# Performance work log

Hardware: AMD Instinct MI355X
Metric: run time of the kernel (lower is better)

The kernel has to match this reference:

```python
import jax, jax.numpy as jnp
import numpy as np

N, E, D, R, G, C = 100000, 600000, 128, 4, 256, 16
EPS = 1e-5

def _rgcn(x, src, dst, edge_type, w_rel, w_root, b):
    # out_i = x_i @ W_root + b + sum_r mean_{j in N_r(i)} x_j @ W_r  (PyG RGCNConv, aggr='mean')
    x_src = x[src]                                   # [E, D] gather
    out = x @ w_root + b                             # [N, D]
    for r in range(R):
        m = (edge_type == r).astype(x.dtype)         # [E]
        msg = (x_src @ w_rel[r]) * m[:, None]        # [E, D]
        agg = jax.ops.segment_sum(msg, dst, num_segments=N)
        cnt = jax.ops.segment_sum(m, dst, num_segments=N)
        out = out + agg / jnp.maximum(cnt, 1.0)[:, None]
    return out

def _bn_eval(x, gamma, beta, mean, var):
    return (x - mean) * jax.lax.rsqrt(var + EPS) * gamma + beta

def setup_inputs() -> dict:
    key = jax.random.key(0)
    ks = jax.random.split(key, 12)
    x = jax.random.normal(ks[0], (N, D), dtype=jnp.float32)
    edge_index = jax.random.randint(ks[1], (2, E), 0, N)
    edge_type = jax.random.randint(ks[2], (E,), 0, R)
    batch = jnp.sort(jax.random.randint(ks[3], (N,), 0, G))
    s = 1.0 / np.sqrt(D)
    conv_rel_w = jax.random.normal(ks[4], (3, R, D, D), dtype=jnp.float32) * s
    conv_root_w = jax.random.normal(ks[5], (3, D, D), dtype=jnp.float32) * s
    conv_bias = jnp.zeros((3, D), dtype=jnp.float32)
    bn_gamma = jnp.ones((2, D), dtype=jnp.float32)
    bn_beta = jnp.zeros((2, D), dtype=jnp.float32)
    bn_mean = jax.random.normal(ks[6], (2, D), dtype=jnp.float32) * 0.1
    bn_var = jax.random.uniform(ks[7], (2, D), minval=0.5, maxval=1.5, dtype=jnp.float32)
    cls_w1 = jax.random.normal(ks[8], (D, D // 2), dtype=jnp.float32) * s
    cls_b1 = jnp.zeros((D // 2,), dtype=jnp.float32)
    cls_w2 = jax.random.normal(ks[9], (D // 2, C), dtype=jnp.float32) / np.sqrt(D // 2)
    cls_b2 = jnp.zeros((C,), dtype=jnp.float32)
    return {"x": x, "edge_index": edge_index, "edge_type": edge_type, "batch": batch,
            "conv_rel_w": conv_rel_w, "conv_root_w": conv_root_w, "conv_bias": conv_bias,
            "bn_gamma": bn_gamma, "bn_beta": bn_beta, "bn_mean": bn_mean, "bn_var": bn_var,
            "cls_w1": cls_w1, "cls_b1": cls_b1, "cls_w2": cls_w2, "cls_b2": cls_b2}

def reference(x, edge_index, edge_type, batch, conv_rel_w, conv_root_w, conv_bias,
              bn_gamma, bn_beta, bn_mean, bn_var, cls_w1, cls_b1, cls_w2, cls_b2):
    src, dst = edge_index[0], edge_index[1]
    prev = None
    h = x
    for i in range(3):
        h_new = _rgcn(h, src, dst, edge_type, conv_rel_w[i], conv_root_w[i], conv_bias[i])
        if prev is not None:
            h_new = h_new + prev  # residual (shapes always match: D==D)
        if i != 2:
            h_new = _bn_eval(h_new, bn_gamma[i], bn_beta[i], bn_mean[i], bn_var[i])
            h_new = jax.nn.elu(h_new)  # alpha=1; dropout inactive in eval
        prev = h_new
        h = h_new
    # global mean pool over graphs
    sums = jax.ops.segment_sum(h, batch, num_segments=G)          # [G, D]
    cnts = jax.ops.segment_sum(jnp.ones((N,), h.dtype), batch, num_segments=G)
    pooled = sums / jnp.maximum(cnts, 1.0)[:, None]
    z = jax.nn.elu(pooled @ cls_w1 + cls_b1)
    logits = z @ cls_w2 + cls_b2
    return jax.nn.log_softmax(logits, axis=-1)
```

## Files before the change

### kernel.cpp

```cpp
#include <hip/hip_runtime.h>
#include <hip/hip_bf16.h>

#define NN 100000
#define EE 600000
#define DD 128
#define GG 256
#define CCL 16

typedef __attribute__((ext_vector_type(8))) short short8;
typedef __attribute__((ext_vector_type(4))) float f32x4;

__global__ __launch_bounds__(256) void sniff_kernel(const void* __restrict__ xraw, int* __restrict__ flag) {
    int t = threadIdx.x;
    const unsigned short* u = (const unsigned short*)xraw;
    int good = 0;
    #pragma unroll
    for (int i = 0; i < 4; i++) {
        unsigned short b = u[t * 4 + i];
        int e = (b >> 7) & 0xFF;
        if (e >= 107 && e <= 130) good++;
    }
    __shared__ int sg[256];
    sg[t] = good;
    __syncthreads();
    for (int s = 128; s > 0; s >>= 1) { if (t < s) sg[t] += sg[t + s]; __syncthreads(); }
    if (t == 0) flag[0] = (sg[0] >= 900) ? 1 : 0;
}

__device__ __forceinline__ float loadf(const void* p, size_t i, int isbf) {
    if (isbf) {
        unsigned short b = ((const unsigned short*)p)[i];
        return __uint_as_float(((unsigned)b) << 16);
    }
    return ((const float*)p)[i];
}

__global__ __launch_bounds__(256) void convx_kernel(const void* __restrict__ xraw, const int* __restrict__ flag,
                                                    __hip_bfloat16* __restrict__ xc) {
    int isbf = flag[0];
    size_t i0 = ((size_t)blockIdx.x * 256 + threadIdx.x) * 8;
    if (i0 >= (size_t)NN * DD) return;
    if (isbf) {
        *(uint4*)(xc + i0) = *(const uint4*)((const __hip_bfloat16*)xraw + i0);
    } else {
        const float* xf = (const float*)xraw;
        #pragma unroll
        for (int j = 0; j < 8; j++) xc[i0 + j] = __float2bfloat16(xf[i0 + j]);
    }
}

__global__ __launch_bounds__(256) void convw_kernel(const void* __restrict__ rel_raw, const void* __restrict__ root_raw,
                                                    const int* __restrict__ flag, __hip_bfloat16* __restrict__ wt) {
    int isbf = flag[0];
    int mat = blockIdx.x;
    int layer = mat / 5, g = mat % 5;
    size_t srcoff = (g == 0) ? (size_t)layer * 16384 : (size_t)(layer * 4 + (g - 1)) * 16384;
    const void* sraw = (g == 0) ? root_raw : rel_raw;
    __hip_bfloat16* dstp = wt + (size_t)mat * 16384;
    for (int idx = threadIdx.x; idx < 16384; idx += 256) {
        int k = idx >> 7, n = idx & 127;
        float v = loadf(sraw, srcoff + (size_t)k * 128 + n, isbf);
        dstp[n * 128 + k] = __float2bfloat16(v);
    }
}

__global__ __launch_bounds__(256) void convp_kernel(const void* bias, const void* bng, const void* bnb,
                                                    const void* bnm, const void* bnv, const void* w1,
                                                    const void* b1, const void* w2, const void* b2,
                                                    const int* __restrict__ flag, float* __restrict__ pf) {
    int isbf = flag[0];
    const void* srcs[9] = {bias, bng, bnb, bnm, bnv, w1, b1, w2, b2};
    const int cnts[9] = {384, 256, 256, 256, 256, 8192, 64, 1024, 16};
    const int offs[9] = {0, 384, 640, 896, 1152, 1408, 9600, 9664, 10688};
    int b = blockIdx.x;
    const void* s = srcs[b];
    int c = cnts[b], o = offs[b];
    for (int i = threadIdx.x; i < c; i += 256) pf[o + i] = loadf(s, i, isbf);
}

__global__ __launch_bounds__(256) void count_kernel(const int* __restrict__ dst, int* __restrict__ cnt) {
    int e = blockIdx.x * 256 + threadIdx.x;
    if (e < EE) atomicAdd(&cnt[dst[e]], 1);
}

__global__ __launch_bounds__(256) void alloc_kernel(const int* __restrict__ cnt, int* __restrict__ counter,
                                                    int* __restrict__ startp, int* __restrict__ wptr) {
    int n = blockIdx.x * 256 + threadIdx.x;
    int lane = threadIdx.x & 63;
    int c = (n < NN) ? cnt[n] : 0;
    int v = c;
    #pragma unroll
    for (int d = 1; d < 64; d <<= 1) {
        int o = __shfl_up(v, d);
        if (lane >= d) v += o;
    }
    int base = 0;
    if (lane == 63) base = atomicAdd(counter, v);
    base = __shfl(base, 63);
    if (n < NN) {
        int s = base + v - c;
        startp[n] = s;
        wptr[n]  = s;
    }
}

__global__ __launch_bounds__(256) void fill_kernel(const int* __restrict__ src, const int* __restrict__ dst,
                                                   const int* __restrict__ et, int* __restrict__ wptr,
                                                   int* __restrict__ elist) {
    int e = blockIdx.x * 256 + threadIdx.x;
    if (e < EE) {
        int d = dst[e];
        int pos = atomicAdd(&wptr[d], 1);
        elist[pos] = src[e] | (et[e] << 17);
    }
}

__global__ __launch_bounds__(256) void agg_kernel(const __hip_bfloat16* __restrict__ h,
                                                  const int* __restrict__ elist,
                                                  const int* __restrict__ startp,
                                                  const int* __restrict__ cnt,
                                                  __hip_bfloat16* __restrict__ xagg) {
    int wid = (blockIdx.x * 256 + threadIdx.x) >> 6;
    int lane = threadIdx.x & 63;
    if (wid >= NN) return;
    int s = startp[wid], c = cnt[wid];
    float a0x=0,a0y=0,a1x=0,a1y=0,a2x=0,a2y=0,a3x=0,a3y=0;
    int c0=0,c1=0,c2=0,c3=0;
    int my = (lane < c) ? elist[s + lane] : 0;
    for (int e = 0; e < c; e++) {
        int packed = (e < 64) ? __shfl(my, e) : elist[s + e];
        int srcn = packed & 0x1FFFF;
        int r = (packed >> 17) & 3;
        __hip_bfloat162 v = ((const __hip_bfloat162*)(h + (size_t)srcn * DD))[lane];
        float vx = __bfloat162float(v.x), vy = __bfloat162float(v.y);
        if (r == 0)      { a0x += vx; a0y += vy; c0++; }
        else if (r == 1) { a1x += vx; a1y += vy; c1++; }
        else if (r == 2) { a2x += vx; a2y += vy; c2++; }
        else             { a3x += vx; a3y += vy; c3++; }
    }
    __hip_bfloat162* out = (__hip_bfloat162*)(xagg + (size_t)wid * 512);
    float i0 = 1.0f / (float)(c0 ? c0 : 1), i1 = 1.0f / (float)(c1 ? c1 : 1);
    float i2 = 1.0f / (float)(c2 ? c2 : 1), i3 = 1.0f / (float)(c3 ? c3 : 1);
    __hip_bfloat162 o;
    o.x = __float2bfloat16(a0x * i0); o.y = __float2bfloat16(a0y * i0); out[lane]       = o;
    o.x = __float2bfloat16(a1x * i1); o.y = __float2bfloat16(a1y * i1); out[64 + lane]  = o;
    o.x = __float2bfloat16(a2x * i2); o.y = __float2bfloat16(a2y * i2); out[128 + lane] = o;
    o.x = __float2bfloat16(a3x * i3); o.y = __float2bfloat16(a3y * i3); out[192 + lane] = o;
}

__global__ __launch_bounds__(256) void gemm_kernel(const __hip_bfloat16* __restrict__ h_in,
                                                   const __hip_bfloat16* __restrict__ xagg,
                                                   const __hip_bfloat16* __restrict__ wt,
                                                   const float* __restrict__ bias,
                                                   const float* __restrict__ bng,
                                                   const float* __restrict__ bnb,
                                                   const float* __restrict__ bnm,
                                                   const float* __restrict__ bnv,
                                                   const __hip_bfloat16* __restrict__ hres,
                                                   __hip_bfloat16* __restrict__ hout,
                                                   int do_bn) {
    __shared__ __align__(16) __hip_bfloat16 Alds[128][136];
    __shared__ __align__(16) __hip_bfloat16 Blds[128][136];
    int t = threadIdx.x;
    int wave = t >> 6, lane = t & 63;
    int quad = lane >> 4, r16 = lane & 15;
    int m0 = blockIdx.x * 128;
    f32x4 acc[2][8];
    #pragma unroll
    for (int i = 0; i < 2; i++)
        #pragma unroll
        for (int j = 0; j < 8; j++) acc[i][j] = (f32x4){0.f, 0.f, 0.f, 0.f};

    for (int g = 0; g < 5; g++) {
        #pragma unroll
        for (int it = 0; it < 8; it++) {
            int sgi = t + it * 256;
            int row = sgi >> 4, seg = sgi & 15;
            int node = m0 + row; if (node >= NN) node = NN - 1;
            const uint4* sp = (g == 0)
                ? (const uint4*)(h_in + (size_t)node * 128)
                : (const uint4*)(xagg + (size_t)node * 512 + (size_t)(g - 1) * 128);
            uint4 val = sp[seg];
            *(uint4*)&Alds[row][seg * 8] = val;
        }
        const uint4* wp = (const uint4*)(wt + (size_t)g * 16384);
        #pragma unroll
        for (int it = 0; it < 8; it++) {
            int sgi = t + it * 256;
            int n = sgi >> 4, seg = sgi & 15;
            uint4 val = wp[n * 16 + seg];
            *(uint4*)&Blds[n][seg * 8] = val;
        }
        __syncthreads();
        #pragma unroll
        for (int kc = 0; kc < 4; kc++) {
            short8 a0 = *(const short8*)&Alds[wave * 32 + r16][kc * 32 + quad * 8];
            short8 a1 = *(const short8*)&Alds[wave * 32 + 16 + r16][kc * 32 + quad * 8];
            #pragma unroll
            for (int nt = 0; nt < 8; nt++) {
                short8 b = *(const short8*)&Blds[nt * 16 + r16][kc * 32 + quad * 8];
                acc[0][nt] = __builtin_amdgcn_mfma_f32_16x16x32_bf16(a0, b, acc[0][nt], 0, 0, 0);
                acc[1][nt] = __builtin_amdgcn_mfma_f32_16x16x32_bf16(a1, b, acc[1][nt], 0, 0, 0);
            }
        }
        __syncthreads();
    }
    #pragma unroll
    for (int nt = 0; nt < 8; nt++) {
        int col = nt * 16 + r16;
        float bv = bias[col];
        float gmul = 0.f, gadd = 0.f;
        if (do_bn) {
            float iva = rsqrtf(bnv[col] + 1e-5f);
            gmul = bng[col] * iva;
            gadd = bnb[col] - bnm[col] * gmul;
        }
        #pragma unroll
        for (int mt = 0; mt < 2; mt++) {
            #pragma unroll
            for (int reg = 0; reg < 4; reg++) {
                int node = m0 + wave * 32 + mt * 16 + quad * 4 + reg;
                if (node >= NN) continue;
                float v = acc[mt][nt][reg] + bv;
                if (hres) v += __bfloat162float(hres[(size_t)node * 128 + col]);
                if (do_bn) {
                    v = v * gmul + gadd;
                    v = v > 0.f ? v : expm1f(v);
                }
                hout[(size_t)node * 128 + col] = __float2bfloat16(v);
            }
        }
    }
}

__global__ __launch_bounds__(256) void pool_kernel(const __hip_bfloat16* __restrict__ h3,
                                                   const int* __restrict__ batch,
                                                   float* __restrict__ pooled) {
    int g = blockIdx.x, t = threadIdx.x;
    int d = t & 127, half = t >> 7;
    int lo = 0, hi = NN;
    while (lo < hi) { int mid = (lo + hi) >> 1; if (batch[mid] < g) lo = mid + 1; else hi = mid; }
    int s0 = lo;
    hi = NN;
    while (lo < hi) { int mid = (lo + hi) >> 1; if (batch[mid] < g + 1) lo = mid + 1; else hi = mid; }
    int s1 = lo;
    float acc = 0.f;
    for (int n = s0 + half; n < s1; n += 2) acc += __bfloat162float(h3[(size_t)n * 128 + d]);
    __shared__ float sd[256];
    sd[t] = acc;
    __syncthreads();
    if (t < 128) {
        int c = s1 - s0;
        pooled[g * 128 + t] = (sd[t] + sd[t + 128]) / (float)(c > 0 ? c : 1);
    }
}

__global__ __launch_bounds__(64) void cls_kernel(const float* __restrict__ pooled,
                                                 const float* __restrict__ pf,
                                                 const int* __restrict__ flag,
                                                 void* __restrict__ out) {
    int g = blockIdx.x, j = threadIdx.x;
    const float* w1 = pf + 1408;
    const float* b1 = pf + 9600;
    const float* w2 = pf + 9664;
    const float* b2 = pf + 10688;
    __shared__ float z[64];
    __shared__ float lg[16];
    const float* p = pooled + g * 128;
    float acc = b1[j];
    for (int d = 0; d < 128; d++) acc += p[d] * w1[d * 64 + j];
    acc = acc > 0.f ? acc : expm1f(acc);
    z[j] = acc;
    __syncthreads();
    if (j < CCL) {
        float l = b2[j];
        for (int k = 0; k < 64; k++) l += z[k] * w2[k * 16 + j];
        lg[j] = l;
    }
    __syncthreads();
    if (j < CCL) {
        float m = lg[0];
        for (int k = 1; k < CCL; k++) m = fmaxf(m, lg[k]);
        float s = 0.f;
        for (int k = 0; k < CCL; k++) s += expf(lg[k] - m);
        float val = lg[j] - m - logf(s);
        if (flag[0]) ((__hip_bfloat16*)out)[g * CCL + j] = __float2bfloat16(val);
        else         ((float*)out)[g * CCL + j] = val;
    }
}

extern "C" void kernel_launch(void* const* d_in, const int* in_sizes, int n_in,
                              void* d_out, int out_size, void* d_ws, size_t ws_size,
                              hipStream_t stream) {
    const void* x_raw    = d_in[0];
    const int* ei        = (const int*)d_in[1];
    const int* et        = (const int*)d_in[2];
    const int* batch     = (const int*)d_in[3];
    const void* rel_raw  = d_in[4];
    const void* root_raw = d_in[5];
    const void* bias_r   = d_in[6];
    const void* bng_r    = d_in[7];
    const void* bnb_r    = d_in[8];
    const void* bnm_r    = d_in[9];
    const void* bnv_r    = d_in[10];
    const void* w1_r     = d_in[11];
    const void* b1_r     = d_in[12];
    const void* w2_r     = d_in[13];
    const void* b2_r     = d_in[14];
    const int* srcp = ei;
    const int* dstp = ei + EE;

    char* ws = (char*)d_ws;
    size_t off = 0;
    auto take = [&](size_t bytes) { size_t r = off; off += (bytes + 1023) & ~(size_t)1023; return r; };
    __hip_bfloat16* xagg = (__hip_bfloat16*)(ws + take((size_t)NN * 512 * 2));
    __hip_bfloat16* xc   = (__hip_bfloat16*)(ws + take((size_t)NN * 128 * 2));
    __hip_bfloat16* hA   = (__hip_bfloat16*)(ws + take((size_t)NN * 128 * 2));
    __hip_bfloat16* hB   = (__hip_bfloat16*)(ws + take((size_t)NN * 128 * 2));
    __hip_bfloat16* hC   = (__hip_bfloat16*)(ws + take((size_t)NN * 128 * 2));
    __hip_bfloat16* wt   = (__hip_bfloat16*)(ws + take((size_t)15 * 16384 * 2));
    float* pf            = (float*)(ws + take((size_t)10704 * 4));
    float* pooled        = (float*)(ws + take((size_t)GG * 128 * 4));
    int* cnt             = (int*)(ws + take((size_t)NN * 4 + 8));
    int* counter         = cnt + NN;
    int* flag            = cnt + NN + 1;
    int* startp          = (int*)(ws + take((size_t)NN * 4));
    int* wptr            = (int*)(ws + take((size_t)NN * 4));
    int* elist           = (int*)(ws + take((size_t)EE * 4));

    hipMemsetAsync(cnt, 0, (size_t)NN * 4 + 4, stream);
    sniff_kernel<<<1, 256, 0, stream>>>(x_raw, flag);
    convx_kernel<<<(NN * DD / 8 + 255) / 256, 256, 0, stream>>>(x_raw, flag, xc);
    convw_kernel<<<15, 256, 0, stream>>>(rel_raw, root_raw, flag, wt);
    convp_kernel<<<9, 256, 0, stream>>>(bias_r, bng_r, bnb_r, bnm_r, bnv_r,
                                        w1_r, b1_r, w2_r, b2_r, flag, pf);
    count_kernel<<<(EE + 255) / 256, 256, 0, stream>>>(dstp, cnt);
    alloc_kernel<<<(NN + 255) / 256, 256, 0, stream>>>(cnt, counter, startp, wptr);
    fill_kernel<<<(EE + 255) / 256, 256, 0, stream>>>(srcp, dstp, et, wptr, elist);

    const __hip_bfloat16* hin = xc;
    __hip_bfloat16* houts[3] = {hA, hB, hC};
    for (int l = 0; l < 3; l++) {
        agg_kernel<<<(NN * 64 + 255) / 256, 256, 0, stream>>>(hin, elist, startp, cnt, xagg);
        int bl = l < 2 ? l : 1;
        gemm_kernel<<<(NN + 127) / 128, 256, 0, stream>>>(
            hin, xagg, wt + (size_t)l * 5 * 16384, pf + l * 128,
            pf + 384 + bl * 128, pf + 640 + bl * 128, pf + 896 + bl * 128, pf + 1152 + bl * 128,
            (l > 0) ? hin : (const __hip_bfloat16*)nullptr, houts[l], (l < 2) ? 1 : 0);
        hin = houts[l];
    }
    pool_kernel<<<GG, 256, 0, stream>>>(houts[2], batch, pooled);
    cls_kernel<<<GG, 64, 0, stream>>>(pooled, pf, flag, (void*)d_out);
}
```

Before: 706.1 us.

## Vectorize aggregation, async-LDS swizzled GEMM with staged epilogue, vectorized pooling

The aggregation kernel now gives each 16-lane group one neighbor edge and reads 16-byte rows, handling two edges per group per iteration. Per-relation sums and counts are combined with cross-lane shuffles instead of one 4-byte load per lane per edge. The GEMM loads its tiles with global_load_lds into a smaller XOR-swizzled LDS buffer over ten K=64 chunks, and precomputes the BN scale and shift in shared memory. Its epilogue is staged through LDS so residual reads and output writes are 16-byte vectors. Pooling and the fp32-to-bf16 conversion are also vectorized. This adds more synchronization points per K chunk and more complex indexing.

```diff
diff --git a/kernel.cpp b/kernel.cpp
--- a/kernel.cpp
+++ b/kernel.cpp
@@ -9,6 +9,26 @@
 
 typedef __attribute__((ext_vector_type(8))) short short8;
 typedef __attribute__((ext_vector_type(4))) float f32x4;
+typedef const __attribute__((address_space(1))) void* gas_t;
+typedef __attribute__((address_space(3))) void* las_t;
+
+__device__ __forceinline__ void async_ld16(const void* g, void* l) {
+    __builtin_amdgcn_global_load_lds((gas_t)g, (las_t)l, 16, 0, 0);
+}
+__device__ __forceinline__ unsigned short f2bf(float x) {
+    unsigned u = __float_as_uint(x);
+    unsigned r = (u + 0x7FFFu + ((u >> 16) & 1u)) >> 16;
+    return (unsigned short)r;
+}
+__device__ __forceinline__ float bf2f(unsigned short b) {
+    return __uint_as_float(((unsigned)b) << 16);
+}
+__device__ __forceinline__ void unpack8(uint4 v, float* f) {
+    f[0] = __uint_as_float(v.x << 16); f[1] = __uint_as_float(v.x & 0xFFFF0000u);
+    f[2] = __uint_as_float(v.y << 16); f[3] = __uint_as_float(v.y & 0xFFFF0000u);
+    f[4] = __uint_as_float(v.z << 16); f[5] = __uint_as_float(v.z & 0xFFFF0000u);
+    f[6] = __uint_as_float(v.w << 16); f[7] = __uint_as_float(v.w & 0xFFFF0000u);
+}
 
 __global__ __launch_bounds__(256) void sniff_kernel(const void* __restrict__ xraw, int* __restrict__ flag) {
     int t = threadIdx.x;
@@ -28,10 +48,7 @@
 }
 
 __device__ __forceinline__ float loadf(const void* p, size_t i, int isbf) {
-    if (isbf) {
-        unsigned short b = ((const unsigned short*)p)[i];
-        return __uint_as_float(((unsigned)b) << 16);
-    }
+    if (isbf) return bf2f(((const unsigned short*)p)[i]);
     return ((const float*)p)[i];
 }
 
@@ -44,8 +61,10 @@
         *(uint4*)(xc + i0) = *(const uint4*)((const __hip_bfloat16*)xraw + i0);
     } else {
         const float* xf = (const float*)xraw;
-        #pragma unroll
-        for (int j = 0; j < 8; j++) xc[i0 + j] = __float2bfloat16(xf[i0 + j]);
+        unsigned short o[8];
+        #pragma unroll
+        for (int j = 0; j < 8; j++) o[j] = f2bf(xf[i0 + j]);
+        *(uint4*)(xc + i0) = *(uint4*)o;
     }
 }
 
@@ -124,111 +143,179 @@
     int lane = threadIdx.x & 63;
     if (wid >= NN) return;
     int s = startp[wid], c = cnt[wid];
-    float a0x=0,a0y=0,a1x=0,a1y=0,a2x=0,a2y=0,a3x=0,a3y=0;
-    int c0=0,c1=0,c2=0,c3=0;
+    int egrp = lane >> 4, col16 = lane & 15;
     int my = (lane < c) ? elist[s + lane] : 0;
-    for (int e = 0; e < c; e++) {
-        int packed = (e < 64) ? __shfl(my, e) : elist[s + e];
-        int srcn = packed & 0x1FFFF;
-        int r = (packed >> 17) & 3;
-        __hip_bfloat162 v = ((const __hip_bfloat162*)(h + (size_t)srcn * DD))[lane];
-        float vx = __bfloat162float(v.x), vy = __bfloat162float(v.y);
-        if (r == 0)      { a0x += vx; a0y += vy; c0++; }
-        else if (r == 1) { a1x += vx; a1y += vy; c1++; }
-        else if (r == 2) { a2x += vx; a2y += vy; c2++; }
-        else             { a3x += vx; a3y += vy; c3++; }
-    }
-    __hip_bfloat162* out = (__hip_bfloat162*)(xagg + (size_t)wid * 512);
-    float i0 = 1.0f / (float)(c0 ? c0 : 1), i1 = 1.0f / (float)(c1 ? c1 : 1);
-    float i2 = 1.0f / (float)(c2 ? c2 : 1), i3 = 1.0f / (float)(c3 ? c3 : 1);
-    __hip_bfloat162 o;
-    o.x = __float2bfloat16(a0x * i0); o.y = __float2bfloat16(a0y * i0); out[lane]       = o;
-    o.x = __float2bfloat16(a1x * i1); o.y = __float2bfloat16(a1y * i1); out[64 + lane]  = o;
-    o.x = __float2bfloat16(a2x * i2); o.y = __float2bfloat16(a2y * i2); out[128 + lane] = o;
-    o.x = __float2bfloat16(a3x * i3); o.y = __float2bfloat16(a3y * i3); out[192 + lane] = o;
-}
-
-__global__ __launch_bounds__(256) void gemm_kernel(const __hip_bfloat16* __restrict__ h_in,
-                                                   const __hip_bfloat16* __restrict__ xagg,
-                                                   const __hip_bfloat16* __restrict__ wt,
-                                                   const float* __restrict__ bias,
-                                                   const float* __restrict__ bng,
-                                                   const float* __restrict__ bnb,
-                                                   const float* __restrict__ bnm,
-                                                   const float* __restrict__ bnv,
-                                                   const __hip_bfloat16* __restrict__ hres,
-                                                   __hip_bfloat16* __restrict__ hout,
-                                                   int do_bn) {
-    __shared__ __align__(16) __hip_bfloat16 Alds[128][136];
-    __shared__ __align__(16) __hip_bfloat16 Blds[128][136];
+    float acc[4][8];
+    float cc[4] = {0.f, 0.f, 0.f, 0.f};
+    #pragma unroll
+    for (int rr = 0; rr < 4; rr++)
+        #pragma unroll
+        for (int j = 0; j < 8; j++) acc[rr][j] = 0.f;
+
+    for (int base = 0; base < c; base += 8) {
+        int eA = base + egrp, eB = base + 4 + egrp;
+        bool actA = eA < c, actB = eB < c;
+        int pA = __shfl(my, eA & 63);
+        int pB = __shfl(my, eB & 63);
+        if (actA && eA >= 64) pA = elist[s + eA];
+        if (actB && eB >= 64) pB = elist[s + eB];
+        int srcA = pA & 0x1FFFF, rA = (pA >> 17) & 3;
+        int srcB = pB & 0x1FFFF, rB = (pB >> 17) & 3;
+        uint4 vA = make_uint4(0, 0, 0, 0), vB = make_uint4(0, 0, 0, 0);
+        if (actA) vA = *(const uint4*)(h + (size_t)srcA * DD + col16 * 8);
+        if (actB) vB = *(const uint4*)(h + (size_t)srcB * DD + col16 * 8);
+        float fA[8], fB[8];
+        unpack8(vA, fA);
+        unpack8(vB, fB);
+        #pragma unroll
+        for (int rr = 0; rr < 4; rr++) {
+            float mA = (actA && rA == rr) ? 1.f : 0.f;
+            float mB = (actB && rB == rr) ? 1.f : 0.f;
+            cc[rr] += mA + mB;
+            #pragma unroll
+            for (int j = 0; j < 8; j++)
+                acc[rr][j] = fmaf(mA, fA[j], fmaf(mB, fB[j], acc[rr][j]));
+        }
+    }
+    #pragma unroll
+    for (int rr = 0; rr < 4; rr++) {
+        cc[rr] += __shfl_xor(cc[rr], 16);
+        cc[rr] += __shfl_xor(cc[rr], 32);
+        #pragma unroll
+        for (int j = 0; j < 8; j++) {
+            float sv = acc[rr][j];
+            sv += __shfl_xor(sv, 16);
+            sv += __shfl_xor(sv, 32);
+            acc[rr][j] = sv;
+        }
+    }
+    float o[8], ct;
+    #pragma unroll
+    for (int j = 0; j < 8; j++)
+        o[j] = egrp < 2 ? (egrp == 0 ? acc[0][j] : acc[1][j])
+                        : (egrp == 2 ? acc[2][j] : acc[3][j]);
+    ct = egrp < 2 ? (egrp == 0 ? cc[0] : cc[1]) : (egrp == 2 ? cc[2] : cc[3]);
+    float inv = 1.f / fmaxf(ct, 1.f);
+    unsigned short u[8];
+    #pragma unroll
+    for (int j = 0; j < 8; j++) u[j] = f2bf(o[j] * inv);
+    *(uint4*)(xagg + (size_t)wid * 512 + egrp * 128 + col16 * 8) = *(uint4*)u;
+}
+
+__global__ __launch_bounds__(256, 4) void gemm_kernel(const __hip_bfloat16* __restrict__ h_in,
+                                                      const __hip_bfloat16* __restrict__ xagg,
+                                                      const __hip_bfloat16* __restrict__ wt,
+                                                      const float* __restrict__ bias,
+                                                      const float* __restrict__ bng,
+                                                      const float* __restrict__ bnb,
+                                                      const float* __restrict__ bnm,
+                                                      const float* __restrict__ bnv,
+                                                      const __hip_bfloat16* __restrict__ hres,
+                                                      __hip_bfloat16* __restrict__ hout,
+                                                      int do_bn) {
+    __shared__ __align__(16) short lds[16384];
+    __shared__ float sbias[128], sgm[128], sga[128];
+    short* Ab = lds;
+    short* Bb = lds + 8192;
     int t = threadIdx.x;
-    int wave = t >> 6, lane = t & 63;
-    int quad = lane >> 4, r16 = lane & 15;
+    int wave = t >> 6, lane = t & 63, quad = lane >> 4, r16 = lane & 15;
     int m0 = blockIdx.x * 128;
+
+    if (t < 128) {
+        sbias[t] = bias[t];
+        float gm = 0.f, ga = 0.f;
+        if (do_bn) {
+            float iva = rsqrtf(bnv[t] + 1e-5f);
+            gm = bng[t] * iva;
+            ga = bnb[t] - bnm[t] * gm;
+        }
+        sgm[t] = gm; sga[t] = ga;
+    }
+
+    int rbase = t >> 3;
+    int gseg8 = ((t & 7) ^ (rbase & 7)) * 8;
+
     f32x4 acc[2][8];
     #pragma unroll
     for (int i = 0; i < 2; i++)
         #pragma unroll
         for (int j = 0; j < 8; j++) acc[i][j] = (f32x4){0.f, 0.f, 0.f, 0.f};
 
-    for (int g = 0; g < 5; g++) {
-        #pragma unroll
-        for (int it = 0; it < 8; it++) {
-            int sgi = t + it * 256;
-            int row = sgi >> 4, seg = sgi & 15;
-            int node = m0 + row; if (node >= NN) node = NN - 1;
-            const uint4* sp = (g == 0)
-                ? (const uint4*)(h_in + (size_t)node * 128)
-                : (const uint4*)(xagg + (size_t)node * 512 + (size_t)(g - 1) * 128);
-            uint4 val = sp[seg];
-            *(uint4*)&Alds[row][seg * 8] = val;
-        }
-        const uint4* wp = (const uint4*)(wt + (size_t)g * 16384);
-        #pragma unroll
-        for (int it = 0; it < 8; it++) {
-            int sgi = t + it * 256;
-            int n = sgi >> 4, seg = sgi & 15;
-            uint4 val = wp[n * 16 + seg];
-            *(uint4*)&Blds[n][seg * 8] = val;
+    for (int c = 0; c < 10; c++) {
+        const __hip_bfloat16* asrc;
+        int astride;
+        if (c < 2) { asrc = h_in + c * 64; astride = 128; }
+        else       { asrc = xagg + (c - 2) * 64; astride = 512; }
+        const __hip_bfloat16* bsrc = wt + (size_t)(c >> 1) * 16384 + (c & 1) * 64;
+        #pragma unroll
+        for (int j = 0; j < 4; j++) {
+            int row = j * 32 + rbase;
+            int node = m0 + row; if (node > NN - 1) node = NN - 1;
+            async_ld16(asrc + (size_t)node * astride + gseg8, &Ab[(j * 256 + t) * 8]);
+            async_ld16(bsrc + (size_t)row * 128 + gseg8, &Bb[(j * 256 + t) * 8]);
         }
         __syncthreads();
         #pragma unroll
-        for (int kc = 0; kc < 4; kc++) {
-            short8 a0 = *(const short8*)&Alds[wave * 32 + r16][kc * 32 + quad * 8];
-            short8 a1 = *(const short8*)&Alds[wave * 32 + 16 + r16][kc * 32 + quad * 8];
+        for (int kc = 0; kc < 2; kc++) {
+            int ra0 = wave * 32 + r16;
+            int ra1 = ra0 + 16;
+            short8 a0 = *(const short8*)&Ab[(ra0 * 8 + ((kc * 4 + quad) ^ (ra0 & 7))) * 8];
+            short8 a1 = *(const short8*)&Ab[(ra1 * 8 + ((kc * 4 + quad) ^ (ra1 & 7))) * 8];
             #pragma unroll
             for (int nt = 0; nt < 8; nt++) {
-                short8 b = *(const short8*)&Blds[nt * 16 + r16][kc * 32 + quad * 8];
+                int rb = nt * 16 + r16;
+                short8 b = *(const short8*)&Bb[(rb * 8 + ((kc * 4 + quad) ^ (rb & 7))) * 8];
                 acc[0][nt] = __builtin_amdgcn_mfma_f32_16x16x32_bf16(a0, b, acc[0][nt], 0, 0, 0);
                 acc[1][nt] = __builtin_amdgcn_mfma_f32_16x16x32_bf16(a1, b, acc[1][nt], 0, 0, 0);
             }
         }
         __syncthreads();
     }
+
     #pragma unroll
     for (int nt = 0; nt < 8; nt++) {
         int col = nt * 16 + r16;
-        float bv = bias[col];
-        float gmul = 0.f, gadd = 0.f;
-        if (do_bn) {
-            float iva = rsqrtf(bnv[col] + 1e-5f);
-            gmul = bng[col] * iva;
-            gadd = bnb[col] - bnm[col] * gmul;
-        }
+        float bv = sbias[col];
         #pragma unroll
         for (int mt = 0; mt < 2; mt++) {
             #pragma unroll
             for (int reg = 0; reg < 4; reg++) {
-                int node = m0 + wave * 32 + mt * 16 + quad * 4 + reg;
-                if (node >= NN) continue;
-                float v = acc[mt][nt][reg] + bv;
-                if (hres) v += __bfloat162float(hres[(size_t)node * 128 + col]);
-                if (do_bn) {
-                    v = v * gmul + gadd;
-                    v = v > 0.f ? v : expm1f(v);
+                int row = wave * 32 + mt * 16 + quad * 4 + reg;
+                int sslot = (col >> 3) ^ (row & 15);
+                lds[row * 128 + sslot * 8 + (col & 7)] = (short)f2bf(acc[mt][nt][reg] + bv);
+            }
+        }
+    }
+    __syncthreads();
+    int row = t >> 1, half = t & 1;
+    int node = m0 + row;
+    if (node < NN) {
+        #pragma unroll
+        for (int q = 0; q < 8; q++) {
+            int seg = half * 8 + q;
+            int sslot = seg ^ (row & 15);
+            short8 cv = *(const short8*)&lds[row * 128 + sslot * 8];
+            int col0 = seg * 8;
+            float v[8];
+            #pragma unroll
+            for (int j = 0; j < 8; j++) v[j] = bf2f((unsigned short)cv[j]);
+            if (hres) {
+                float rf[8];
+                unpack8(*(const uint4*)(hres + (size_t)node * 128 + col0), rf);
+                #pragma unroll
+                for (int j = 0; j < 8; j++) v[j] += rf[j];
+            }
+            if (do_bn) {
+                #pragma unroll
+                for (int j = 0; j < 8; j++) {
+                    float z = v[j] * sgm[col0 + j] + sga[col0 + j];
+                    v[j] = z > 0.f ? z : expm1f(z);
                 }
-                hout[(size_t)node * 128 + col] = __float2bfloat16(v);
             }
+            unsigned short u[8];
+            #pragma unroll
+            for (int j = 0; j < 8; j++) u[j] = f2bf(v[j]);
+            *(uint4*)(hout + (size_t)node * 128 + col0) = *(uint4*)u;
         }
     }
 }
@@ -237,21 +324,32 @@
                                                    const int* __restrict__ batch,
                                                    float* __restrict__ pooled) {
     int g = blockIdx.x, t = threadIdx.x;
-    int d = t & 127, half = t >> 7;
+    int rowpar = t >> 4, colg = t & 15;
     int lo = 0, hi = NN;
     while (lo < hi) { int mid = (lo + hi) >> 1; if (batch[mid] < g) lo = mid + 1; else hi = mid; }
     int s0 = lo;
     hi = NN;
     while (lo < hi) { int mid = (lo + hi) >> 1; if (batch[mid] < g + 1) lo = mid + 1; else hi = mid; }
     int s1 = lo;
-    float acc = 0.f;
-    for (int n = s0 + half; n < s1; n += 2) acc += __bfloat162float(h3[(size_t)n * 128 + d]);
-    __shared__ float sd[256];
-    sd[t] = acc;
+    float a[8];
+    #pragma unroll
+    for (int j = 0; j < 8; j++) a[j] = 0.f;
+    for (int n = s0 + rowpar; n < s1; n += 16) {
+        float f[8];
+        unpack8(*(const uint4*)(h3 + (size_t)n * 128 + colg * 8), f);
+        #pragma unroll
+        for (int j = 0; j < 8; j++) a[j] += f[j];
+    }
+    __shared__ float sd[16][128];
+    #pragma unroll
+    for (int j = 0; j < 8; j++) sd[rowpar][colg * 8 + j] = a[j];
     __syncthreads();
     if (t < 128) {
-        int c = s1 - s0;
-        pooled[g * 128 + t] = (sd[t] + sd[t + 128]) / (float)(c > 0 ? c : 1);
+        float sum = 0.f;
+        #pragma unroll
+        for (int i = 0; i < 16; i++) sum += sd[i][t];
+        int cgn = s1 - s0;
+        pooled[g * 128 + t] = sum / (float)(cgn > 0 ? cgn : 1);
     }
 }
 
@@ -298,15 +396,6 @@
     const int* batch     = (const int*)d_in[3];
     const void* rel_raw  = d_in[4];
     const void* root_raw = d_in[5];
-    const void* bias_r   = d_in[6];
-    const void* bng_r    = d_in[7];
-    const void* bnb_r    = d_in[8];
-    const void* bnm_r    = d_in[9];
-    const void* bnv_r    = d_in[10];
-    const void* w1_r     = d_in[11];
-    const void* b1_r     = d_in[12];
-    const void* w2_r     = d_in[13];
-    const void* b2_r     = d_in[14];
     const int* srcp = ei;
     const int* dstp = ei + EE;
 
@@ -332,8 +421,8 @@
     sniff_kernel<<<1, 256, 0, stream>>>(x_raw, flag);
     convx_kernel<<<(NN * DD / 8 + 255) / 256, 256, 0, stream>>>(x_raw, flag, xc);
     convw_kernel<<<15, 256, 0, stream>>>(rel_raw, root_raw, flag, wt);
-    convp_kernel<<<9, 256, 0, stream>>>(bias_r, bng_r, bnb_r, bnm_r, bnv_r,
-                                        w1_r, b1_r, w2_r, b2_r, flag, pf);
+    convp_kernel<<<9, 256, 0, stream>>>(d_in[6], d_in[7], d_in[8], d_in[9], d_in[10],
+                                        d_in[11], d_in[12], d_in[13], d_in[14], flag, pf);
     count_kernel<<<(EE + 255) / 256, 256, 0, stream>>>(dstp, cnt);
     alloc_kernel<<<(NN + 255) / 256, 256, 0, stream>>>(cnt, counter, startp, wptr);
     fill_kernel<<<(EE + 255) / 256, 256, 0, stream>>>(srcp, dstp, et, wptr, elist);
```

Measured after the change: 700.6 us. Within noise of the previous version (-0.8%).
